# Kernel tuning notes

Hardware: AMD Instinct MI355X
Metric: run time of the kernel (lower is better)

The kernel has to match this reference:

```python
import jax, jax.numpy as jnp
import numpy as np

B, S, D, H = 4, 1024, 1024, 16
HD = D // H  # head_dim = 64


def setup_inputs() -> dict:
    key = jax.random.key(0)
    k1, k2, k3, k4 = jax.random.split(key, 4)
    scale = 1.0 / np.sqrt(D)
    return {
        "x": jax.random.normal(k1, (B, S, D), dtype=jnp.float32),
        "w_qkv": jax.random.normal(k2, (3 * D, D), dtype=jnp.float32) * scale,
        "w_out": jax.random.normal(k3, (D, D), dtype=jnp.float32) * scale,
        "b_out": jax.random.normal(k4, (D,), dtype=jnp.float32) * scale,
    }


def reference(x, w_qkv, w_out, b_out):
    b, s, d_model = x.shape
    # qkv linear (no bias): (b, s, 3*D); torch Linear computes x @ W.T
    qkv = x @ w_qkv.T
    # Rearrange 'b s (qkv h hd) -> qkv b h s hd'
    qkv = qkv.reshape(b, s, 3, H, HD).transpose(2, 0, 3, 1, 4)
    q, k, v = qkv[0], qkv[1], qkv[2]
    scale = HD ** -0.5
    att = jax.nn.softmax(jnp.einsum('bhxd,bhyd->bhxy', q, k) * scale, axis=-1)
    out = jnp.einsum('bhxy,bhyd->bhxd', att, v)  # (b, h, s, hd)
    out = out.transpose(0, 2, 1, 3).reshape(b, s, d_model)  # 'b h s hd -> b s (h hd)'
    return out @ w_out.T + b_out
```

## Files before the change

kernel.cpp:

```cpp
#include <hip/hip_runtime.h>
#include <hip/hip_bf16.h>
#include <stdint.h>

typedef unsigned short u16;
typedef __bf16 bf16x8 __attribute__((ext_vector_type(8)));
typedef u16 u16x8 __attribute__((ext_vector_type(8)));
typedef u16 u16x4 __attribute__((ext_vector_type(4)));
typedef float f32x4 __attribute__((ext_vector_type(4)));

#define MFMA_16x16x32(a, b, c) __builtin_amdgcn_mfma_f32_16x16x32_bf16((a), (b), (c), 0, 0, 0)

#if __has_builtin(__builtin_amdgcn_exp2f)
#define EXP2F(x) __builtin_amdgcn_exp2f(x)
#else
#define EXP2F(x) exp2f(x)
#endif

#define QSCALE_F 0.18033688011112042f

__device__ __forceinline__ u16 f2b(float f) {
  __bf16 h = (__bf16)f;
  return __builtin_bit_cast(u16, h);
}

__device__ __forceinline__ void store_c(u16* C, size_t idx, float v) { C[idx] = f2b(v); }
__device__ __forceinline__ void store_c(float* C, size_t idx, float v) { C[idx] = v; }

__device__ __forceinline__ void gload16(const void* g, void* l) {
  __builtin_amdgcn_global_load_lds(
      (const __attribute__((address_space(1))) unsigned int*)(uintptr_t)(g),
      (__attribute__((address_space(3))) unsigned int*)(uintptr_t)(l),
      16, 0, 0);
}

template <int N> __device__ __forceinline__ void wait_vmcnt();
#define DEF_WAITVM(N)                                          \
  template <> __device__ __forceinline__ void wait_vmcnt<N>() { \
    asm volatile("s_waitcnt vmcnt(" #N ")" ::: "memory");       \
    __builtin_amdgcn_sched_barrier(0);                          \
  }
DEF_WAITVM(0) DEF_WAITVM(3) DEF_WAITVM(4) DEF_WAITVM(5) DEF_WAITVM(8)

__device__ __forceinline__ void wait_lgkm0() {
  asm volatile("s_waitcnt lgkmcnt(0)" ::: "memory");
  __builtin_amdgcn_sched_barrier(0);
}

template <typename T, int ROWS>
__device__ __forceinline__ void stage_tile(const T* __restrict__ G, int ldg, int tr, int k0,
                                           T* Ls, int wave, int lane) {
  constexpr int EPL = 16 / sizeof(T);
  constexpr int PCE = 64 * EPL;
  constexpr int CALLS = (ROWS * 32) / (4 * PCE);
#pragma unroll
  for (int ci = 0; ci < CALLS; ci++) {
    const int base = (wave * CALLS + ci) * PCE;
    const int idx0 = base + lane * EPL;
    const int r = idx0 >> 5;
    const int c = idx0 & 31;
    int csw;
    if constexpr (sizeof(T) == 2)
      csw = ((c >> 3) ^ (r & 3)) << 3;
    else
      csw = ((c >> 2) ^ (r & 7)) << 2;
    gload16(G + (size_t)(tr + r) * ldg + k0 + csw, Ls + base);
  }
}
template <typename T, int ROWS>
struct stage_calls {
  static constexpr int value = (ROWS * 32) / (4 * 64 * (16 / (int)sizeof(T)));
};

__device__ __forceinline__ bf16x8 load_frag_sw(const u16* Ls, int row, int g8) {
  const int c = ((g8 >> 3) ^ (row & 3)) << 3;
  return *(const bf16x8*)(Ls + row * 32 + c);
}
__device__ __forceinline__ bf16x8 load_frag_sw(const float* Ls, int row, int g8) {
  const int g2 = g8 >> 2;
  const int c0 = (g2 ^ (row & 7)) << 2;
  const int c1 = ((g2 + 1) ^ (row & 7)) << 2;
  f32x4 lo = *(const f32x4*)(Ls + row * 32 + c0);
  f32x4 hi = *(const f32x4*)(Ls + row * 32 + c1);
  bf16x8 r;
#pragma unroll
  for (int e = 0; e < 4; e++) {
    r[e] = (__bf16)lo[e];
    r[e + 4] = (__bf16)hi[e];
  }
  return r;
}

template <typename TA, typename TB, typename TC, bool BIAS, bool QSC, int TM>
__global__ __launch_bounds__(256, 2) void gemm_bt(const TA* __restrict__ A,
                                                  const TB* __restrict__ B,
                                                  const float* __restrict__ bias,
                                                  TC* __restrict__ C,
                                                  int M, int N, int K) {
  constexpr int MI = TM >> 5;
  constexpr int NL = stage_calls<TA, TM>::value + stage_calls<TB, 128>::value;
  __shared__ TA As[2][TM * 32];
  __shared__ TB Bs[2][128 * 32];
  const int tid = threadIdx.x;
  const int lane = tid & 63;
  const int wave = tid >> 6;
  const int l15 = lane & 15;
  const int g = lane >> 4;
  const int g8 = g * 8;
  const int cpx = (int)gridDim.x >> 3;
  const int xsl = (int)blockIdx.x & 7;
  const int jj = (int)blockIdx.x >> 3;
  const int tiles_n = N >> 7;
  int tmi, tni;
  const int gm = cpx / tiles_n;
  if (gm * tiles_n == cpx) {
    tmi = xsl * gm + (jj % gm);
    tni = jj / gm;
  } else {
    const int bid = xsl * cpx + jj;
    tmi = bid / tiles_n;
    tni = bid % tiles_n;
  }
  const int tm = tmi * TM;
  const int tn = tni << 7;
  const int wm = (wave >> 1) * (TM >> 1);
  const int wn = (wave & 1) << 6;

  f32x4 acc[MI][4] = {};

  const int nt = K >> 5;
  stage_tile<TA, TM>(A, K, tm, 0, As[0], wave, lane);
  stage_tile<TB, 128>(B, K, tn, 0, Bs[0], wave, lane);

  for (int t = 0; t < nt; t++) {
    const int cur = t & 1;
    if (t + 1 < nt) {
      stage_tile<TA, TM>(A, K, tm, (t + 1) << 5, As[cur ^ 1], wave, lane);
      stage_tile<TB, 128>(B, K, tn, (t + 1) << 5, Bs[cur ^ 1], wave, lane);
      wait_vmcnt<NL>();
    } else {
      wait_vmcnt<0>();
    }
    __builtin_amdgcn_s_barrier();
    __builtin_amdgcn_sched_barrier(0);
    bf16x8 af[MI], bfr[4];
#pragma unroll
    for (int i = 0; i < MI; i++) af[i] = load_frag_sw(As[cur], wm + i * 16 + l15, g8);
#pragma unroll
    for (int i = 0; i < 4; i++) bfr[i] = load_frag_sw(Bs[cur], wn + i * 16 + l15, g8);
    wait_lgkm0();
    __builtin_amdgcn_s_barrier();
#pragma unroll
    for (int mi = 0; mi < MI; mi++)
#pragma unroll
      for (int nj = 0; nj < 4; nj++)
        acc[mi][nj] = MFMA_16x16x32(af[mi], bfr[nj], acc[mi][nj]);
  }

  float bv[4], cs[4];
#pragma unroll
  for (int nj = 0; nj < 4; nj++) {
    const int col = tn + wn + nj * 16 + l15;
    bv[nj] = BIAS ? bias[col] : 0.0f;
    cs[nj] = (QSC && col < 1024) ? QSCALE_F : 1.0f;
  }

#pragma unroll
  for (int mi = 0; mi < MI; mi++) {
#pragma unroll
    for (int nj = 0; nj < 4; nj++) {
      const int row = tm + wm + mi * 16 + g * 4;
      const int col = tn + wn + nj * 16 + l15;
#pragma unroll
      for (int r = 0; r < 4; r++)
        store_c(C, (size_t)(row + r) * N + col, (acc[mi][nj][r] + bv[nj]) * cs[nj]);
    }
  }
}

__global__ __launch_bounds__(256) void cvt3(const float* __restrict__ x,
                                            const float* __restrict__ wq,
                                            const float* __restrict__ wo,
                                            u16* __restrict__ xb,
                                            u16* __restrict__ wqb,
                                            u16* __restrict__ wob) {
  const int i = blockIdx.x * 256 + threadIdx.x;
  const float* src;
  u16* dst;
  int k;
  if (i < 524288) {
    src = x;
    dst = xb;
    k = i;
  } else if (i < 524288 + 393216) {
    src = wq;
    dst = wqb;
    k = i - 524288;
  } else {
    src = wo;
    dst = wob;
    k = i - (524288 + 393216);
  }
  const f32x4* p = (const f32x4*)src + (size_t)k * 2;
  f32x4 a = p[0], bq = p[1];
  u16x8 r;
#pragma unroll
  for (int e = 0; e < 4; e++) {
    r[e] = f2b(a[e]);
    r[e + 4] = f2b(bq[e]);
  }
  *((u16x8*)dst + k) = r;
}

__global__ __launch_bounds__(256) void cvt_bf16(const float* __restrict__ in,
                                                u16* __restrict__ out, int n8) {
  const int i = blockIdx.x * 256 + threadIdx.x;
  if (i >= n8) return;
  const f32x4* p = (const f32x4*)in + (size_t)i * 2;
  f32x4 a = p[0], b = p[1];
  u16x8 r;
#pragma unroll
  for (int e = 0; e < 4; e++) {
    r[e] = f2b(a[e]);
    r[e + 4] = f2b(b[e]);
  }
  *((u16x8*)out + i) = r;
}

__device__ __forceinline__ int swz64(int row) { return ((row >> 3) ^ row) & 7; }

__global__ __launch_bounds__(512) void attn(const u16* __restrict__ qkv,
                                            u16* __restrict__ attout) {
  __shared__ u16 Ks[4][64 * 64];
  __shared__ u16 Vs[4][64 * 64];
  __shared__ u16 Pl[8][32 * 64];
  const int tid = threadIdx.x;
  const int lane = tid & 63;
  const int w = tid >> 6;
  const int l15 = lane & 15;
  const int g = lane >> 4;
  const int g8 = g * 8;

  const int bid = blockIdx.x;
  const int xs = bid & 7;
  const int j = bid >> 3;
  const int bh = xs * 8 + (j >> 2);
  const int qt = j & 3;
  const int b = bh >> 4;
  const int h = bh & 15;
  const size_t rowbase = (size_t)b * 1024;
  const int qcol = h * 64;

  const int qr0 = qt * 256 + w * 32;
  bf16x8 qf[2][2];
#pragma unroll
  for (int mi = 0; mi < 2; mi++)
#pragma unroll
    for (int ks = 0; ks < 2; ks++)
      qf[mi][ks] =
          *(const bf16x8*)&qkv[(rowbase + qr0 + mi * 16 + l15) * 3072 + qcol + ks * 32 + g8];

  f32x4 o[2][4] = {};
  float l_r[2][4] = {};

  const int vh3 = tid & 7;
  const int vhc = vh3 << 3;
  const int vkey = tid >> 3;
  bf16x8 vreg[2];

  auto loadV = [&](int kt, int vr) {
    vreg[vr] = *(const bf16x8*)&qkv[(rowbase + kt * 64 + vkey) * 3072 + 2048 + qcol + vhc];
  };
  auto writeV = [&](int buf, int vr) {
    const int pos = ((vkey & 15) << 2) | (vkey >> 4);
    const u16* vu = (const u16*)&vreg[vr];
#pragma unroll
    for (int e = 0; e < 8; e++) {
      const int sl = (vh3 ^ e) & 7;
      Vs[buf][(vhc + e) * 64 + (pos ^ (sl << 3))] = vu[e];
    }
  };
  auto stageK = [&](int buf, int kt) {
    const int row = w * 8 + (lane >> 3);
    const int cc = (lane & 7) ^ swz64(row);
    gload16(&qkv[(rowbase + kt * 64 + row) * 3072 + 1024 + qcol + cc * 8],
            &Ks[buf][w * 512]);
  };

  auto compute = [&](int buf) {
    f32x4 s[2][4] = {};
    __builtin_amdgcn_s_setprio(1);
#pragma unroll
    for (int nj = 0; nj < 4; nj++) {
      const int key = nj * 16 + l15;
      const int sk = swz64(key) << 3;
#pragma unroll
      for (int ks = 0; ks < 2; ks++) {
        const bf16x8 kfr = *(const bf16x8*)&Ks[buf][key * 64 + ((ks * 32 + g8) ^ sk)];
#pragma unroll
        for (int mi = 0; mi < 2; mi++)
          s[mi][nj] = MFMA_16x16x32(qf[mi][ks], kfr, s[mi][nj]);
      }
    }
    __builtin_amdgcn_s_setprio(0);
#pragma unroll
    for (int mi = 0; mi < 2; mi++)
#pragma unroll
      for (int r = 0; r < 4; r++) {
        const float p0 = EXP2F(s[mi][0][r]);
        const float p1 = EXP2F(s[mi][1][r]);
        const float p2 = EXP2F(s[mi][2][r]);
        const float p3 = EXP2F(s[mi][3][r]);
        l_r[mi][r] += (p0 + p1) + (p2 + p3);
        const int row = mi * 16 + g * 4 + r;
        const int sq = swz64(row) << 3;
        u16x4 pk;
        pk[0] = f2b(p0);
        pk[1] = f2b(p1);
        pk[2] = f2b(p2);
        pk[3] = f2b(p3);
        *(u16x4*)&Pl[w][row * 64 + ((l15 << 2) ^ sq)] = pk;
      }
    bf16x8 pf[2][2];
#pragma unroll
    for (int mi = 0; mi < 2; mi++) {
      const int pr = mi * 16 + l15;
      const int sp = swz64(pr) << 3;
#pragma unroll
      for (int ks = 0; ks < 2; ks++)
        pf[mi][ks] = *(const bf16x8*)&Pl[w][pr * 64 + ((ks * 32 + g8) ^ sp)];
    }
    __builtin_amdgcn_s_setprio(1);
#pragma unroll
    for (int nj = 0; nj < 4; nj++) {
      const int hd = nj * 16 + l15;
      const int sv = swz64(hd) << 3;
#pragma unroll
      for (int ks = 0; ks < 2; ks++) {
        const bf16x8 vf = *(const bf16x8*)&Vs[buf][hd * 64 + ((ks * 32 + g8) ^ sv)];
#pragma unroll
        for (int mi = 0; mi < 2; mi++)
          o[mi][nj] = MFMA_16x16x32(pf[mi][ks], vf, o[mi][nj]);
      }
    }
    __builtin_amdgcn_s_setprio(0);
  };

  stageK(0, 0);
  stageK(1, 1);
  loadV(0, 0);
  loadV(1, 1);
  writeV(0, 0);
  writeV(1, 1);
  __syncthreads();

  for (int kt2 = 0; kt2 < 8; kt2++) {
    const int t0 = kt2 * 2;
    if (kt2 < 7) {
      stageK((t0 + 2) & 3, t0 + 2);
      stageK((t0 + 3) & 3, t0 + 3);
      loadV(t0 + 2, 0);
      loadV(t0 + 3, 1);
    }
    compute(t0 & 3);
    compute((t0 + 1) & 3);
    if (kt2 < 7) {
      writeV((t0 + 2) & 3, 0);
      writeV((t0 + 3) & 3, 1);
    }
    __syncthreads();
  }

#pragma unroll
  for (int mi = 0; mi < 2; mi++)
#pragma unroll
    for (int r = 0; r < 4; r++) {
      float v = l_r[mi][r];
#pragma unroll
      for (int d = 1; d < 16; d <<= 1) v += __shfl_xor(v, d, 64);
      l_r[mi][r] = v;
    }

#pragma unroll
  for (int mi = 0; mi < 2; mi++) {
    float inv[4];
#pragma unroll
    for (int r = 0; r < 4; r++) inv[r] = 1.0f / l_r[mi][r];
#pragma unroll
    for (int nj = 0; nj < 4; nj++)
#pragma unroll
      for (int r = 0; r < 4; r++)
        attout[(rowbase + qr0 + mi * 16 + g * 4 + r) * 1024 + qcol + nj * 16 + l15] =
            f2b(o[mi][nj][r] * inv[r]);
  }
}

extern "C" void kernel_launch(void* const* d_in, const int* in_sizes, int n_in,
                              void* d_out, int out_size, void* d_ws, size_t ws_size,
                              hipStream_t stream) {
  const float* x = (const float*)d_in[0];
  const float* w_qkv = (const float*)d_in[1];
  const float* w_out = (const float*)d_in[2];
  const float* b_out = (const float*)d_in[3];
  float* out = (float*)d_out;

  u16* qkv = (u16*)d_ws;
  u16* attout = qkv + 12582912;
  const size_t needA = 39845888ull;
  const size_t needB = needA + 2097152ull;

  u16* xb = attout;
  u16* wqb = attout + 4194304;

  if (ws_size >= needB) {
    u16* wob = wqb + 3145728;
    cvt3<<<dim3(4096), dim3(256), 0, stream>>>(x, w_qkv, w_out, xb, wqb, wob);
    gemm_bt<u16, u16, u16, false, true, 128><<<dim3(32 * 24), dim3(256), 0, stream>>>(
        xb, wqb, nullptr, qkv, 4096, 3072, 1024);
    attn<<<dim3(256), dim3(512), 0, stream>>>(qkv, attout);
    gemm_bt<u16, u16, float, true, false, 64><<<dim3(64 * 8), dim3(256), 0, stream>>>(
        attout, wob, b_out, out, 4096, 1024, 1024);
  } else if (ws_size >= needA) {
    u16* wob = wqb;
    cvt3<<<dim3(3584), dim3(256), 0, stream>>>(x, w_qkv, w_qkv, xb, wqb, wob);
    gemm_bt<u16, u16, u16, false, true, 128><<<dim3(32 * 24), dim3(256), 0, stream>>>(
        xb, wqb, nullptr, qkv, 4096, 3072, 1024);
    cvt_bf16<<<dim3(512), dim3(256), 0, stream>>>(w_out, wob, 131072);
    attn<<<dim3(256), dim3(512), 0, stream>>>(qkv, attout);
    gemm_bt<u16, u16, float, true, false, 64><<<dim3(64 * 8), dim3(256), 0, stream>>>(
        attout, wob, b_out, out, 4096, 1024, 1024);
  } else {
    gemm_bt<float, float, u16, false, true, 128><<<dim3(32 * 24), dim3(256), 0, stream>>>(
        x, w_qkv, nullptr, qkv, 4096, 3072, 1024);
    attn<<<dim3(256), dim3(512), 0, stream>>>(qkv, attout);
    gemm_bt<u16, float, float, true, false, 64><<<dim3(64 * 8), dim3(256), 0, stream>>>(
        attout, w_out, b_out, out, 4096, 1024, 1024);
  }
}
```

Measured before the change: 88.39 us.

## Process two K-tiles per barrier pair with four-stage LDS ring in GEMM

The GEMM main loop now stages two 32-wide K tiles per iteration into a four-buffer LDS ring and handles both per barrier pair. This halves the number of barriers and vmcnt waits per K step and raises the MFMA work between synchronisations. In exchange LDS use doubles and more fragment registers are live, which may cut occupancy below the two blocks per CU set by the launch bounds. It assumes K is a multiple of 64, and the wait count of 2*NL requires matching DEF_WAITVM specialisations.

```diff
diff --git a/kernel.cpp b/kernel.cpp
--- a/kernel.cpp
+++ b/kernel.cpp
@@ -39,7 +39,8 @@
     asm volatile("s_waitcnt vmcnt(" #N ")" ::: "memory");       \
     __builtin_amdgcn_sched_barrier(0);                          \
   }
-DEF_WAITVM(0) DEF_WAITVM(3) DEF_WAITVM(4) DEF_WAITVM(5) DEF_WAITVM(8)
+DEF_WAITVM(0) DEF_WAITVM(4) DEF_WAITVM(5) DEF_WAITVM(6) DEF_WAITVM(8)
+DEF_WAITVM(10) DEF_WAITVM(16)
 
 __device__ __forceinline__ void wait_lgkm0() {
   asm volatile("s_waitcnt lgkmcnt(0)" ::: "memory");
@@ -98,8 +99,8 @@
                                                   int M, int N, int K) {
   constexpr int MI = TM >> 5;
   constexpr int NL = stage_calls<TA, TM>::value + stage_calls<TB, 128>::value;
-  __shared__ TA As[2][TM * 32];
-  __shared__ TB Bs[2][128 * 32];
+  __shared__ TA As[4][TM * 32];
+  __shared__ TB Bs[4][128 * 32];
   const int tid = threadIdx.x;
   const int lane = tid & 63;
   const int wave = tid >> 6;
@@ -127,33 +128,47 @@
 
   f32x4 acc[MI][4] = {};
 
-  const int nt = K >> 5;
+  const int np = K >> 6;
   stage_tile<TA, TM>(A, K, tm, 0, As[0], wave, lane);
   stage_tile<TB, 128>(B, K, tn, 0, Bs[0], wave, lane);
-
-  for (int t = 0; t < nt; t++) {
-    const int cur = t & 1;
-    if (t + 1 < nt) {
-      stage_tile<TA, TM>(A, K, tm, (t + 1) << 5, As[cur ^ 1], wave, lane);
-      stage_tile<TB, 128>(B, K, tn, (t + 1) << 5, Bs[cur ^ 1], wave, lane);
-      wait_vmcnt<NL>();
+  stage_tile<TA, TM>(A, K, tm, 32, As[1], wave, lane);
+  stage_tile<TB, 128>(B, K, tn, 32, Bs[1], wave, lane);
+
+  for (int p = 0; p < np; p++) {
+    const int t0 = p * 2;
+    const int bA = t0 & 3;
+    const int bB = (t0 + 1) & 3;
+    if (p + 1 < np) {
+      stage_tile<TA, TM>(A, K, tm, (t0 + 2) << 5, As[(t0 + 2) & 3], wave, lane);
+      stage_tile<TB, 128>(B, K, tn, (t0 + 2) << 5, Bs[(t0 + 2) & 3], wave, lane);
+      stage_tile<TA, TM>(A, K, tm, (t0 + 3) << 5, As[(t0 + 3) & 3], wave, lane);
+      stage_tile<TB, 128>(B, K, tn, (t0 + 3) << 5, Bs[(t0 + 3) & 3], wave, lane);
+      wait_vmcnt<2 * NL>();
     } else {
       wait_vmcnt<0>();
     }
     __builtin_amdgcn_s_barrier();
     __builtin_amdgcn_sched_barrier(0);
-    bf16x8 af[MI], bfr[4];
-#pragma unroll
-    for (int i = 0; i < MI; i++) af[i] = load_frag_sw(As[cur], wm + i * 16 + l15, g8);
-#pragma unroll
-    for (int i = 0; i < 4; i++) bfr[i] = load_frag_sw(Bs[cur], wn + i * 16 + l15, g8);
+    bf16x8 af[2][MI], bfr[2][4];
+#pragma unroll
+    for (int i = 0; i < MI; i++) {
+      af[0][i] = load_frag_sw(As[bA], wm + i * 16 + l15, g8);
+      af[1][i] = load_frag_sw(As[bB], wm + i * 16 + l15, g8);
+    }
+#pragma unroll
+    for (int i = 0; i < 4; i++) {
+      bfr[0][i] = load_frag_sw(Bs[bA], wn + i * 16 + l15, g8);
+      bfr[1][i] = load_frag_sw(Bs[bB], wn + i * 16 + l15, g8);
+    }
     wait_lgkm0();
     __builtin_amdgcn_s_barrier();
 #pragma unroll
-    for (int mi = 0; mi < MI; mi++)
-#pragma unroll
-      for (int nj = 0; nj < 4; nj++)
-        acc[mi][nj] = MFMA_16x16x32(af[mi], bfr[nj], acc[mi][nj]);
+    for (int h = 0; h < 2; h++)
+#pragma unroll
+      for (int mi = 0; mi < MI; mi++)
+#pragma unroll
+        for (int nj = 0; nj < 4; nj++)
+          acc[mi][nj] = MFMA_16x16x32(af[h][mi], bfr[h][nj], acc[mi][nj]);
   }
 
   float bv[4], cs[4];
```

New measurement: 88.37 us. No clear change (-0.0%).
